# Kernel tuning notes

Hardware: AMD Instinct MI355X
Metric: run time of the kernel (lower is better)

Reference implementation:

```python
import jax, jax.numpy as jnp
import numpy as np

EPS = 1e-5  # BatchNorm eps (torch default)


def _coords():
    # coord_tensor[i] = [(i//5 - 2)/2, (i%5 - 2)/2] for 5x5 grid of 25 objects
    i = jnp.arange(25)
    return jnp.stack([(i // 5 - 2) / 2.0, (i % 5 - 2) / 2.0], axis=-1).astype(jnp.float32)


def _conv_bn(x, w, b, gamma, beta):
    # conv stride2 pad1 -> relu -> batchnorm (training-mode batch stats, as torch module default)
    y = jax.lax.conv_general_dilated(x, w, (2, 2), ((1, 1), (1, 1)),
                                     dimension_numbers=('NCHW', 'OIHW', 'NCHW'))
    y = jax.nn.relu(y + b[None, :, None, None])
    m = y.mean(axis=(0, 2, 3), keepdims=True)
    v = y.var(axis=(0, 2, 3), keepdims=True)
    return gamma[None, :, None, None] * (y - m) * jax.lax.rsqrt(v + EPS) + beta[None, :, None, None]


def setup_inputs() -> dict:
    key = jax.random.key(0)
    ks = iter(jax.random.split(key, 64))
    def rn(shape, scale=0.05):
        return jax.random.normal(next(ks), shape, jnp.float32) * scale
    B = 256
    inp = {
        'x': jax.random.normal(next(ks), (B, 3, 80, 80), jnp.float32),
        'qst': jax.random.normal(next(ks), (B, 11), jnp.float32),
    }
    for l, (ci, co) in enumerate([(3, 24), (24, 24), (24, 24), (24, 24)], 1):
        inp[f'cw{l}'] = rn((co, ci, 3, 3))
        inp[f'cb{l}'] = jnp.zeros((co,), jnp.float32)
        inp[f'bg{l}'] = jnp.ones((co,), jnp.float32)
        inp[f'bb{l}'] = jnp.zeros((co,), jnp.float32)
    for l, (di, do) in enumerate([(63, 256), (256, 256), (256, 256), (256, 256)], 1):
        inp[f'gw{l}'] = rn((di, do))
        inp[f'gb{l}'] = jnp.zeros((do,), jnp.float32)
    for l, (di, do) in enumerate([(256, 256), (256, 256), (256, 10)], 1):
        inp[f'fw{l}'] = rn((di, do))
        inp[f'fb{l}'] = jnp.zeros((do,), jnp.float32)
    return inp


def _forward(x, qst, cw1, cb1, bg1, bb1, cw2, cb2, bg2, bb2,
             cw3, cb3, bg3, bb3, cw4, cb4, bg4, bb4,
             gw1, gb1, gw2, gb2, gw3, gb3, gw4, gb4,
             fw1, fb1, fw2, fb2, fw3, fb3):
    B = x.shape[0]
    # Convolution stack: (B,3,80,80) -> (B,24,5,5)
    h = _conv_bn(x, cw1, cb1, bg1, bb1)
    h = _conv_bn(h, cw2, cb2, bg2, bb2)
    h = _conv_bn(h, cw3, cb3, bg3, bb3)
    h = _conv_bn(h, cw4, cb4, bg4, bb4)
    # Objects: (B,24,25) -> (B,25,24) -> concat coords -> (B,25,26)
    obj = h.reshape(B, 24, 25).transpose(0, 2, 1)
    obj = jnp.concatenate([obj, jnp.broadcast_to(_coords()[None], (B, 25, 2))], axis=-1)
    # Pairwise broadcast-concat: cat([x_i, x_j, qst]) with x_i[b,p,q]=obj[b,q], x_j[b,p,q]=obj[b,p]
    xi = jnp.broadcast_to(obj[:, None, :, :], (B, 25, 25, 26))
    xj = jnp.broadcast_to(obj[:, :, None, :], (B, 25, 25, 26))
    qb = jnp.broadcast_to(qst[:, None, None, :], (B, 25, 25, 11))
    pairs = jnp.concatenate([xi, xj, qb], axis=-1).reshape(B, 625, 63)
    g = jax.nn.relu(pairs @ gw1 + gb1)
    g = jax.nn.relu(g @ gw2 + gb2)
    g = jax.nn.relu(g @ gw3 + gb3)
    g = jax.nn.relu(g @ gw4 + gb4).sum(axis=1)  # (B,256)
    # f_phi (dropout treated as identity for a deterministic reference)
    f = jax.nn.relu(g @ fw1 + fb1)
    f = jax.nn.relu(f @ fw2 + fb2)
    logits = f @ fw3 + fb3
    return jax.nn.log_softmax(logits, axis=1)


def reference(x, qst, cw1, cb1, bg1, bb1, cw2, cb2, bg2, bb2,
              cw3, cb3, bg3, bb3, cw4, cb4, bg4, bb4,
              gw1, gb1, gw2, gb2, gw3, gb3, gw4, gb4,
              fw1, fb1, fw2, fb2, fw3, fb3):
    return _forward(x, qst, cw1, cb1, bg1, bb1, cw2, cb2, bg2, bb2,
                    cw3, cb3, bg3, bb3, cw4, cb4, bg4, bb4,
                    gw1, gb1, gw2, gb2, gw3, gb3, gw4, gb4,
                    fw1, fb1, fw2, fb2, fw3, fb3)
```

## Files before the change

kernel.cpp:

```cpp
#include <hip/hip_runtime.h>
#include <hip/hip_bf16.h>


typedef __attribute__((ext_vector_type(8))) short short8;
typedef __attribute__((ext_vector_type(4))) float floatx4;

__device__ __forceinline__ unsigned short f2bf(float v){
  union { float f; unsigned int u; } c; c.f = v;
  unsigned int u = c.u;
  u += 0x7FFFu + ((u >> 16) & 1u);
  return (unsigned short)(u >> 16);
}

__global__ __launch_bounds__(256) void prep_w_zero(
    const float* __restrict__ gw2, const float* __restrict__ gw3,
    const float* __restrict__ gw4, unsigned short* __restrict__ wf,
    float* __restrict__ stats)
{
  const int bid = blockIdx.x, tid = threadIdx.x;
  if (bid == 0){ for (int j = tid; j < 1536; j += 256) stats[j] = 0.f; }
  const int w = bid >> 8;
  const float* gw = (w == 0) ? gw2 : (w == 1) ? gw3 : gw4;
  const int idx = (bid & 255)*256 + tid;
  const int i = idx & 7, lane = (idx >> 3) & 63, t = (idx >> 9) & 15, kk = idx >> 13;
  const int k = kk*32 + (lane >> 4)*8 + i;
  const int c = t*16 + (lane & 15);
  wf[w*65536 + idx] = f2bf(gw[k*256 + c]);
}

template<int CI, int COG>
__global__ __launch_bounds__(256) void conv_relu_stats(
    const float* __restrict__ in,
    const float* __restrict__ stats_in, const float* __restrict__ gprev,
    const float* __restrict__ bprev, float invN,
    const float* __restrict__ cw, const float* __restrict__ cb,
    float* __restrict__ out, float* __restrict__ stats_out,
    int H, int W, int OH, int OW)
{
  const int co0 = blockIdx.y * COG;
  __shared__ float ssm[2*CI];
  __shared__ float psum[4][COG], psum2[4][COG];
  const int tid = threadIdx.x;
  if (tid < CI){
    if (stats_in){
      float S = 0.f, S2 = 0.f;
      #pragma unroll
      for (int sh = 0; sh < 8; sh++){ S += stats_in[sh*48 + tid]; S2 += stats_in[sh*48 + 24 + tid]; }
      const float mean = S*invN;
      const float var  = S2*invN - mean*mean;
      const float rs   = rsqrtf(var + 1e-5f);
      const float sc   = gprev[tid]*rs;
      ssm[tid] = sc; ssm[CI + tid] = bprev[tid] - mean*sc;
    } else { ssm[tid] = 1.f; ssm[CI + tid] = 0.f; }
  }
  __syncthreads();
  const int idx = blockIdx.x*256 + tid;
  const int ow = idx % OW; const int t2 = idx / OW;
  const int oh = t2 % OH;  const int b  = t2 / OH;
  const float* cwb = cw + co0*CI*9;
  float accv[COG];
  #pragma unroll
  for (int g = 0; g < COG; g++) accv[g] = cb[co0 + g];
  for (int ci = 0; ci < CI; ci++){
    const float* ip = in + ((long)(b*CI + ci))*H*W;
    const float sc = ssm[ci], sh2 = ssm[CI + ci];
    #pragma unroll
    for (int kh = 0; kh < 3; kh++){
      const int ih = oh*2 - 1 + kh;
      if ((unsigned)ih >= (unsigned)H) continue;
      #pragma unroll
      for (int kw = 0; kw < 3; kw++){
        const int iw = ow*2 - 1 + kw;
        if ((unsigned)iw >= (unsigned)W) continue;
        const float v = ip[ih*W + iw]*sc + sh2;
        #pragma unroll
        for (int g = 0; g < COG; g++)
          accv[g] += v * cwb[(g*CI + ci)*9 + kh*3 + kw];
      }
    }
  }
  const int wave = tid >> 6, lane = tid & 63;
  #pragma unroll
  for (int g = 0; g < COG; g++){
    const float v = fmaxf(accv[g], 0.f);
    accv[g] = v;
    out[(((long)b*24 + co0 + g)*OH + oh)*OW + ow] = v;
  }
  #pragma unroll
  for (int g = 0; g < COG; g++){
    float s = accv[g], s2 = accv[g]*accv[g];
    for (int off = 32; off; off >>= 1){ s += __shfl_down(s, off); s2 += __shfl_down(s2, off); }
    if (lane == 0){ psum[wave][g] = s; psum2[wave][g] = s2; }
  }
  __syncthreads();
  if (tid < COG){
    const float S  = psum[0][tid] + psum[1][tid] + psum[2][tid] + psum[3][tid];
    const float S2 = psum2[0][tid] + psum2[1][tid] + psum2[2][tid] + psum2[3][tid];
    const int sh = blockIdx.x & 7;
    atomicAdd(&stats_out[sh*48 + co0 + tid],      S);
    atomicAdd(&stats_out[sh*48 + 24 + co0 + tid], S2);
  }
}

__global__ __launch_bounds__(512) void g_mega(
    const float* __restrict__ y4, const float* __restrict__ stats4,
    const float* __restrict__ bg4, const float* __restrict__ bb4,
    const float* __restrict__ qst, const float* __restrict__ gw1,
    const float* __restrict__ gb1,
    const unsigned short* __restrict__ Wf,
    const float* __restrict__ gb2, const float* __restrict__ gb3, const float* __restrict__ gb4,
    const float* __restrict__ fw1, const float* __restrict__ fb1,
    const float* __restrict__ fw2, const float* __restrict__ fb2,
    const float* __restrict__ fw3, const float* __restrict__ fb3,
    float* __restrict__ out)
{
  __shared__ __align__(16) short act[128*256];
  __shared__ __align__(16) float A_lds[25][260];
  __shared__ __align__(16) float Bm_lds[25][260];
  __shared__ float obj[25][26];
  __shared__ float ssm[48];
  __shared__ float scratch[512];
  __shared__ __align__(16) float bufA[256], bufB[256];
  __shared__ float lg[10];

  const int b = blockIdx.x, tid = threadIdx.x;
  char* actB = (char*)act;
  const int wave = tid >> 6, lane = tid & 63;
  const int lmod = lane & 15, ldiv = lane >> 4;
  const int wm = wave >> 2, wn = wave & 3;

  if (tid < 24){
    float S = 0.f, S2 = 0.f;
    #pragma unroll
    for (int sh = 0; sh < 8; sh++){ S += stats4[sh*48 + tid]; S2 += stats4[sh*48 + 24 + tid]; }
    const float mean = S*(1.f/6400.f);
    const float var  = S2*(1.f/6400.f) - mean*mean;
    const float rs   = rsqrtf(var + 1e-5f);
    const float sc   = bg4[tid]*rs;
    ssm[tid] = sc; ssm[24 + tid] = bb4[tid] - mean*sc;
  }
  __syncthreads();
  for (int j = tid; j < 600; j += 512){
    const int q = j/24, c = j%24;
    obj[q][c] = ssm[c]*y4[((long)(b*24 + c))*25 + q] + ssm[24 + c];
  }
  if (tid < 50){
    const int q = tid >> 1;
    obj[q][24 + (tid & 1)] = (tid & 1) ? (float)(q%5 - 2)*0.5f : (float)(q/5 - 2)*0.5f;
  }
  __syncthreads();
  {
    const int n = tid & 255, half = tid >> 8;
    float wa[26], wb[26];
    #pragma unroll
    for (int c = 0; c < 26; c++){ wa[c] = gw1[c*256 + n]; wb[c] = gw1[(26 + c)*256 + n]; }
    float qv = gb1[n];
    #pragma unroll
    for (int j = 0; j < 11; j++) qv += qst[b*11 + j]*gw1[(52 + j)*256 + n];
    const int q0 = half ? 13 : 0, q1 = half ? 25 : 13;
    for (int q = q0; q < q1; q++){
      float a = qv, bm = 0.f;
      #pragma unroll
      for (int c = 0; c < 26; c++){ const float o = obj[q][c]; a += o*wa[c]; bm += o*wb[c]; }
      A_lds[q][n] = a; Bm_lds[q][n] = bm;
    }
  }
  __syncthreads();

  float gsum = 0.f;
  for (int blk = 0; blk < 5; blk++){
    const int rowbase = blk * 128;
    const int nrows = min(128, 625 - rowbase);
    {
      const int r  = tid >> 2;
      const int q4 = tid & 3;
      if (r < nrows){
        const int row = rowbase + r;
        const float* ap = &A_lds [row % 25][q4*4];
        const float* bp = &Bm_lds[row / 25][q4*4];
        #pragma unroll
        for (int j = 0; j < 16; j++){
          const int c = j*16;
          floatx4 av = *(const floatx4*)(ap + c);
          floatx4 bv = *(const floatx4*)(bp + c);
          unsigned int p0 = (unsigned int)f2bf(fmaxf(av.x+bv.x, 0.f))
                          | ((unsigned int)f2bf(fmaxf(av.y+bv.y, 0.f)) << 16);
          unsigned int p1 = (unsigned int)f2bf(fmaxf(av.z+bv.z, 0.f))
                          | ((unsigned int)f2bf(fmaxf(av.w+bv.w, 0.f)) << 16);
          const int byte = (r*512 + (c + q4*4)*2) ^ ((r & 7) << 4);
          *(uint2*)(actB + byte) = make_uint2(p0, p1);
        }
      } else {
        #pragma unroll
        for (int j = 0; j < 16; j++){
          const int byte = (r*512 + (j*16 + q4*4)*2) ^ ((r & 7) << 4);
          *(uint2*)(actB + byte) = make_uint2(0u, 0u);
        }
      }
    }
    __syncthreads();

    for (int L = 0; L < 3; L++){
      floatx4 acc[4][4];
      #pragma unroll
      for (int m = 0; m < 4; m++)
        #pragma unroll
        for (int n = 0; n < 4; n++)
          acc[m][n] = (floatx4){0.f,0.f,0.f,0.f};
      const short8* wlayer = (const short8*)Wf + (long)L*8192;
      #pragma unroll
      for (int kk = 0; kk < 8; kk++){
        short8 bf[4];
        #pragma unroll
        for (int n = 0; n < 4; n++)
          bf[n] = wlayer[(kk*16 + wn*4 + n)*64 + lane];
        short8 af[4];
        #pragma unroll
        for (int m = 0; m < 4; m++){
          const int arow  = wm*64 + m*16 + lmod;
          const int abyte = (arow*512 + kk*64 + ldiv*16) ^ ((arow & 7) << 4);
          af[m] = *(const short8*)(actB + abyte);
        }
        #pragma unroll
        for (int n = 0; n < 4; n++)
          #pragma unroll
          for (int m = 0; m < 4; m++)
            acc[m][n] = __builtin_amdgcn_mfma_f32_16x16x32_bf16(af[m], bf[n], acc[m][n], 0, 0, 0);
      }

      if (L < 2){
        const float* bias = (L == 0) ? gb2 : gb3;
        __syncthreads();
        #pragma unroll
        for (int n = 0; n < 4; n++){
          const int c = (wn*4 + n)*16 + lmod;
          const float bv = bias[c];
          #pragma unroll
          for (int m = 0; m < 4; m++){
            #pragma unroll
            for (int i = 0; i < 4; i++){
              const int row = wm*64 + m*16 + ldiv*4 + i;
              const float v = fmaxf(acc[m][n][i] + bv, 0.f);
              const int byte = (row*512 + c*2) ^ ((row & 7) << 4);
              *(short*)(actB + byte) = (short)f2bf(v);
            }
          }
        }
        __syncthreads();
      } else {
        __syncthreads();
        #pragma unroll
        for (int n = 0; n < 4; n++){
          const int c = (wn*4 + n)*16 + lmod;
          const float bv = gb4[c];
          float sv = 0.f;
          #pragma unroll
          for (int m = 0; m < 4; m++){
            #pragma unroll
            for (int i = 0; i < 4; i++){
              const int row = wm*64 + m*16 + ldiv*4 + i;
              const float v = fmaxf(acc[m][n][i] + bv, 0.f);
              if (row < nrows) sv += v;
            }
          }
          sv += __shfl_xor(sv, 16);
          sv += __shfl_xor(sv, 32);
          if (ldiv == 0) scratch[wm*256 + c] = sv;
        }
        __syncthreads();
        if (tid < 256) gsum += scratch[tid] + scratch[256 + tid];
      }
    }
  }

  if (tid < 256) bufA[tid] = gsum;
  __syncthreads();
  const int n = tid & 255;
  float acc = 0.f;
  if (tid < 256){
    acc = fb1[n];
    const float4* pa = (const float4*)bufA;
    #pragma unroll 8
    for (int k4 = 0; k4 < 64; k4++){
      const float4 a = pa[k4];
      acc += a.x*fw1[(k4*4 + 0)*256 + n];
      acc += a.y*fw1[(k4*4 + 1)*256 + n];
      acc += a.z*fw1[(k4*4 + 2)*256 + n];
      acc += a.w*fw1[(k4*4 + 3)*256 + n];
    }
    bufB[n] = fmaxf(acc, 0.f);
  }
  __syncthreads();
  if (tid < 256){
    acc = fb2[n];
    const float4* pb = (const float4*)bufB;
    #pragma unroll 8
    for (int k4 = 0; k4 < 64; k4++){
      const float4 a = pb[k4];
      acc += a.x*fw2[(k4*4 + 0)*256 + n];
      acc += a.y*fw2[(k4*4 + 1)*256 + n];
      acc += a.z*fw2[(k4*4 + 2)*256 + n];
      acc += a.w*fw2[(k4*4 + 3)*256 + n];
    }
  }
  __syncthreads();
  if (tid < 256) bufA[n] = fmaxf(acc, 0.f);
  __syncthreads();
  if (tid < 10){
    float a3 = fb3[tid];
    for (int k = 0; k < 256; k++) a3 += bufA[k]*fw3[k*10 + tid];
    lg[tid] = a3;
  }
  __syncthreads();
  if (tid < 10){
    float m = lg[0];
    #pragma unroll
    for (int j = 1; j < 10; j++) m = fmaxf(m, lg[j]);
    float s = 0.f;
    #pragma unroll
    for (int j = 0; j < 10; j++) s += expf(lg[j] - m);
    out[b*10 + tid] = lg[tid] - m - logf(s);
  }
}

extern "C" void kernel_launch(void* const* d_in, const int* in_sizes, int n_in,
                              void* d_out, int out_size, void* d_ws, size_t ws_size,
                              hipStream_t stream)
{
  const float* x   = (const float*)d_in[0];
  const float* qst = (const float*)d_in[1];
  const float* cw1 = (const float*)d_in[2];
  const float* cb1 = (const float*)d_in[3];
  const float* bg1 = (const float*)d_in[4];
  const float* bb1 = (const float*)d_in[5];
  const float* cw2 = (const float*)d_in[6];
  const float* cb2 = (const float*)d_in[7];
  const float* bg2 = (const float*)d_in[8];
  const float* bb2 = (const float*)d_in[9];
  const float* cw3 = (const float*)d_in[10];
  const float* cb3 = (const float*)d_in[11];
  const float* bg3 = (const float*)d_in[12];
  const float* bb3 = (const float*)d_in[13];
  const float* cw4 = (const float*)d_in[14];
  const float* cb4 = (const float*)d_in[15];
  const float* bg4 = (const float*)d_in[16];
  const float* bb4 = (const float*)d_in[17];
  const float* gw1 = (const float*)d_in[18];
  const float* gb1 = (const float*)d_in[19];
  const float* gw2 = (const float*)d_in[20];
  const float* gb2 = (const float*)d_in[21];
  const float* gw3 = (const float*)d_in[22];
  const float* gb3 = (const float*)d_in[23];
  const float* gw4 = (const float*)d_in[24];
  const float* gb4 = (const float*)d_in[25];
  const float* fw1 = (const float*)d_in[26];
  const float* fb1 = (const float*)d_in[27];
  const float* fw2 = (const float*)d_in[28];
  const float* fb2 = (const float*)d_in[29];
  const float* fw3 = (const float*)d_in[30];
  const float* fb3 = (const float*)d_in[31];

  float* wsf    = (float*)d_ws;
  unsigned short* Wf = (unsigned short*)(wsf + 65728);
  float* stats  = wsf + 164032;
  float* y1     = wsf + 240832;
  float* y2     = wsf + 10071232;
  float* y3     = wsf + 12528832;
  float* y4     = wsf + 13143232;

  prep_w_zero<<<768, 256, 0, stream>>>(gw2, gw3, gw4, Wf, stats);
  conv_relu_stats<3,24><<<dim3(1600,1), 256, 0, stream>>>(x, nullptr, nullptr, nullptr, 0.f,
                                               cw1, cb1, y1, stats + 0, 80,80,40,40);
  conv_relu_stats<24,8><<<dim3(400,3), 256, 0, stream>>>(y1, stats + 0, bg1, bb1, 1.f/409600.f,
                                               cw2, cb2, y2, stats + 384, 40,40,20,20);
  conv_relu_stats<24,8><<<dim3(100,3), 256, 0, stream>>>(y2, stats + 384, bg2, bb2, 1.f/102400.f,
                                               cw3, cb3, y3, stats + 768, 20,20,10,10);
  conv_relu_stats<24,8><<<dim3(25,3), 256, 0, stream>>>(y3, stats + 768, bg3, bb3, 1.f/25600.f,
                                              cw4, cb4, y4, stats + 1152, 10,10,5,5);
  g_mega<<<256, 512, 0, stream>>>(y4, stats + 1152, bg4, bb4, qst, gw1, gb1, Wf,
                                  gb2, gb3, gb4, fw1, fb1, fw2, fb2, fw3, fb3,
                                  (float*)d_out);
}
```

Baseline: 293.0 us.

## Fuse weight prep into conv1 and replace atomic BN stats with per-block partials

The bf16 weight-packing kernel and the first convolution now run as one launch, with blocks split by index. This removes one kernel launch and the separate zeroing of the stats buffer. BatchNorm statistics are no longer accumulated with sharded atomics. Each block writes its own partial sums, and every consumer block reduces all partials for the 48 sum/sumsq entries before normalising. The trade-off is that each conv2 block must read and sum 1600 partials per channel entry using only 48 threads. That adds serial L2 traffic and latency to the start of every consumer block.

Measured after the change: 326.3 us. 11.4% more time.

```diff
diff --git a/kernel.cpp b/kernel.cpp
--- a/kernel.cpp
+++ b/kernel.cpp
@@ -12,46 +12,98 @@
   return (unsigned short)(u >> 16);
 }
 
-__global__ __launch_bounds__(256) void prep_w_zero(
+__global__ __launch_bounds__(256) void prep_conv1(
     const float* __restrict__ gw2, const float* __restrict__ gw3,
     const float* __restrict__ gw4, unsigned short* __restrict__ wf,
-    float* __restrict__ stats)
+    const float* __restrict__ x, const float* __restrict__ cw1,
+    const float* __restrict__ cb1,
+    float* __restrict__ out, float* __restrict__ pstats1)
 {
   const int bid = blockIdx.x, tid = threadIdx.x;
-  if (bid == 0){ for (int j = tid; j < 1536; j += 256) stats[j] = 0.f; }
-  const int w = bid >> 8;
-  const float* gw = (w == 0) ? gw2 : (w == 1) ? gw3 : gw4;
-  const int idx = (bid & 255)*256 + tid;
-  const int i = idx & 7, lane = (idx >> 3) & 63, t = (idx >> 9) & 15, kk = idx >> 13;
-  const int k = kk*32 + (lane >> 4)*8 + i;
-  const int c = t*16 + (lane & 15);
-  wf[w*65536 + idx] = f2bf(gw[k*256 + c]);
+  if (bid < 768){
+    const int w = bid >> 8;
+    const float* gw = (w == 0) ? gw2 : (w == 1) ? gw3 : gw4;
+    const int idx = (bid & 255)*256 + tid;
+    const int i = idx & 7, lane = (idx >> 3) & 63, t = (idx >> 9) & 15, kk = idx >> 13;
+    const int k = kk*32 + (lane >> 4)*8 + i;
+    const int c = t*16 + (lane & 15);
+    wf[w*65536 + idx] = f2bf(gw[k*256 + c]);
+    return;
+  }
+  __shared__ float psum[4][24], psum2[4][24];
+  const int cbid = bid - 768;
+  const int idx = cbid*256 + tid;
+  const int ow = idx % 40; const int t2 = idx / 40;
+  const int oh = t2 % 40;  const int b  = idx / 1600;
+  float accv[24];
+  #pragma unroll
+  for (int g = 0; g < 24; g++) accv[g] = cb1[g];
+  for (int ci = 0; ci < 3; ci++){
+    const float* ip = x + ((long)(b*3 + ci))*6400;
+    #pragma unroll
+    for (int kh = 0; kh < 3; kh++){
+      const int ih = oh*2 - 1 + kh;
+      if ((unsigned)ih >= 80u) continue;
+      #pragma unroll
+      for (int kw = 0; kw < 3; kw++){
+        const int iw = ow*2 - 1 + kw;
+        if ((unsigned)iw >= 80u) continue;
+        const float v = ip[ih*80 + iw];
+        #pragma unroll
+        for (int g = 0; g < 24; g++)
+          accv[g] += v * cw1[(g*3 + ci)*9 + kh*3 + kw];
+      }
+    }
+  }
+  const int wave = tid >> 6, lane = tid & 63;
+  #pragma unroll
+  for (int g = 0; g < 24; g++){
+    const float v = fmaxf(accv[g], 0.f);
+    accv[g] = v;
+    out[(((long)b*24 + g)*40 + oh)*40 + ow] = v;
+  }
+  #pragma unroll
+  for (int g = 0; g < 24; g++){
+    float s = accv[g], s2 = accv[g]*accv[g];
+    for (int off = 32; off; off >>= 1){ s += __shfl_down(s, off); s2 += __shfl_down(s2, off); }
+    if (lane == 0){ psum[wave][g] = s; psum2[wave][g] = s2; }
+  }
+  __syncthreads();
+  if (tid < 24){
+    pstats1[tid*1600 + cbid]      = psum[0][tid] + psum[1][tid] + psum[2][tid] + psum[3][tid];
+    pstats1[(24+tid)*1600 + cbid] = psum2[0][tid] + psum2[1][tid] + psum2[2][tid] + psum2[3][tid];
+  }
 }
 
-template<int CI, int COG>
+template<int CI, int COG, int NIN, int NOUT>
 __global__ __launch_bounds__(256) void conv_relu_stats(
-    const float* __restrict__ in,
-    const float* __restrict__ stats_in, const float* __restrict__ gprev,
-    const float* __restrict__ bprev, float invN,
+    const float* __restrict__ in, const float* __restrict__ pst_in,
+    const float* __restrict__ gprev, const float* __restrict__ bprev, float invN,
     const float* __restrict__ cw, const float* __restrict__ cb,
-    float* __restrict__ out, float* __restrict__ stats_out,
+    float* __restrict__ out, float* __restrict__ pst_out,
     int H, int W, int OH, int OW)
 {
   const int co0 = blockIdx.y * COG;
+  __shared__ float ssum[48];
   __shared__ float ssm[2*CI];
   __shared__ float psum[4][COG], psum2[4][COG];
   const int tid = threadIdx.x;
-  if (tid < CI){
-    if (stats_in){
-      float S = 0.f, S2 = 0.f;
-      #pragma unroll
-      for (int sh = 0; sh < 8; sh++){ S += stats_in[sh*48 + tid]; S2 += stats_in[sh*48 + 24 + tid]; }
-      const float mean = S*invN;
-      const float var  = S2*invN - mean*mean;
-      const float rs   = rsqrtf(var + 1e-5f);
-      const float sc   = gprev[tid]*rs;
-      ssm[tid] = sc; ssm[CI + tid] = bprev[tid] - mean*sc;
-    } else { ssm[tid] = 1.f; ssm[CI + tid] = 0.f; }
+  if (tid < 48){
+    float S = 0.f;
+    const float* p = pst_in + tid*NIN;
+    for (int j = 0; j < NIN; j += 4){
+      const float4 v = *(const float4*)(p + j);
+      S += v.x + v.y + v.z + v.w;
+    }
+    ssum[tid] = S;
+  }
+  __syncthreads();
+  if (tid < 24){
+    const float mean = ssum[tid]*invN;
+    const float var  = ssum[24 + tid]*invN - mean*mean;
+    const float rs   = rsqrtf(var + 1e-5f);
+    const float sc   = gprev[tid]*rs;
+    ssm[tid] = sc; ssm[CI + tid] = bprev[tid] - mean*sc;
   }
   __syncthreads();
   const int idx = blockIdx.x*256 + tid;
@@ -94,16 +146,13 @@
   }
   __syncthreads();
   if (tid < COG){
-    const float S  = psum[0][tid] + psum[1][tid] + psum[2][tid] + psum[3][tid];
-    const float S2 = psum2[0][tid] + psum2[1][tid] + psum2[2][tid] + psum2[3][tid];
-    const int sh = blockIdx.x & 7;
-    atomicAdd(&stats_out[sh*48 + co0 + tid],      S);
-    atomicAdd(&stats_out[sh*48 + 24 + co0 + tid], S2);
+    pst_out[(co0 + tid)*NOUT + blockIdx.x]      = psum[0][tid] + psum[1][tid] + psum[2][tid] + psum[3][tid];
+    pst_out[(24 + co0 + tid)*NOUT + blockIdx.x] = psum2[0][tid] + psum2[1][tid] + psum2[2][tid] + psum2[3][tid];
   }
 }
 
 __global__ __launch_bounds__(512) void g_mega(
-    const float* __restrict__ y4, const float* __restrict__ stats4,
+    const float* __restrict__ y4, const float* __restrict__ pstats4,
     const float* __restrict__ bg4, const float* __restrict__ bb4,
     const float* __restrict__ qst, const float* __restrict__ gw1,
     const float* __restrict__ gb1,
@@ -118,6 +167,7 @@
   __shared__ __align__(16) float A_lds[25][260];
   __shared__ __align__(16) float Bm_lds[25][260];
   __shared__ float obj[25][26];
+  __shared__ float ssum[48];
   __shared__ float ssm[48];
   __shared__ float scratch[512];
   __shared__ __align__(16) float bufA[256], bufB[256];
@@ -129,12 +179,17 @@
   const int lmod = lane & 15, ldiv = lane >> 4;
   const int wm = wave >> 2, wn = wave & 3;
 
+  if (tid < 48){
+    float S = 0.f;
+    const float* p = pstats4 + tid*25;
+    #pragma unroll
+    for (int j = 0; j < 25; j++) S += p[j];
+    ssum[tid] = S;
+  }
+  __syncthreads();
   if (tid < 24){
-    float S = 0.f, S2 = 0.f;
-    #pragma unroll
-    for (int sh = 0; sh < 8; sh++){ S += stats4[sh*48 + tid]; S2 += stats4[sh*48 + 24 + tid]; }
-    const float mean = S*(1.f/6400.f);
-    const float var  = S2*(1.f/6400.f) - mean*mean;
+    const float mean = ssum[tid]*(1.f/6400.f);
+    const float var  = ssum[24 + tid]*(1.f/6400.f) - mean*mean;
     const float rs   = rsqrtf(var + 1e-5f);
     const float sc   = bg4[tid]*rs;
     ssm[tid] = sc; ssm[24 + tid] = bb4[tid] - mean*sc;
@@ -360,24 +415,25 @@
   const float* fw3 = (const float*)d_in[30];
   const float* fb3 = (const float*)d_in[31];
 
-  float* wsf    = (float*)d_ws;
+  float* wsf     = (float*)d_ws;
+  float* pstats2 = wsf + 0;
+  float* pstats3 = wsf + 19200;
+  float* pstats4 = wsf + 24000;
   unsigned short* Wf = (unsigned short*)(wsf + 65728);
-  float* stats  = wsf + 164032;
-  float* y1     = wsf + 240832;
-  float* y2     = wsf + 10071232;
-  float* y3     = wsf + 12528832;
-  float* y4     = wsf + 13143232;
-
-  prep_w_zero<<<768, 256, 0, stream>>>(gw2, gw3, gw4, Wf, stats);
-  conv_relu_stats<3,24><<<dim3(1600,1), 256, 0, stream>>>(x, nullptr, nullptr, nullptr, 0.f,
-                                               cw1, cb1, y1, stats + 0, 80,80,40,40);
-  conv_relu_stats<24,8><<<dim3(400,3), 256, 0, stream>>>(y1, stats + 0, bg1, bb1, 1.f/409600.f,
-                                               cw2, cb2, y2, stats + 384, 40,40,20,20);
-  conv_relu_stats<24,8><<<dim3(100,3), 256, 0, stream>>>(y2, stats + 384, bg2, bb2, 1.f/102400.f,
-                                               cw3, cb3, y3, stats + 768, 20,20,10,10);
-  conv_relu_stats<24,8><<<dim3(25,3), 256, 0, stream>>>(y3, stats + 768, bg3, bb3, 1.f/25600.f,
-                                              cw4, cb4, y4, stats + 1152, 10,10,5,5);
-  g_mega<<<256, 512, 0, stream>>>(y4, stats + 1152, bg4, bb4, qst, gw1, gb1, Wf,
+  float* pstats1 = wsf + 164032;
+  float* y1      = wsf + 240832;
+  float* y2      = wsf + 10071232;
+  float* y3      = wsf + 12528832;
+  float* y4      = wsf + 13143232;
+
+  prep_conv1<<<2368, 256, 0, stream>>>(gw2, gw3, gw4, Wf, x, cw1, cb1, y1, pstats1);
+  conv_relu_stats<24,8,1600,400><<<dim3(400,3), 256, 0, stream>>>(
+      y1, pstats1, bg1, bb1, 1.f/409600.f, cw2, cb2, y2, pstats2, 40,40,20,20);
+  conv_relu_stats<24,8,400,100><<<dim3(100,3), 256, 0, stream>>>(
+      y2, pstats2, bg2, bb2, 1.f/102400.f, cw3, cb3, y3, pstats3, 20,20,10,10);
+  conv_relu_stats<24,8,100,25><<<dim3(25,3), 256, 0, stream>>>(
+      y3, pstats3, bg3, bb3, 1.f/25600.f, cw4, cb4, y4, pstats4, 10,10,5,5);
+  g_mega<<<256, 512, 0, stream>>>(y4, pstats4, bg4, bb4, qst, gw1, gb1, Wf,
                                   gb2, gb3, gb4, fw1, fb1, fw2, fb2, fw3, fb3,
                                   (float*)d_out);
 }
```
